# Performance work log

Measured on AMD Instinct MI355X. Metric: run time of the kernel, lower is better.

## Reference

```python
import jax, jax.numpy as jnp
import numpy as np

L, WIDTH, H, B, S = 3, 4, 512, 32, 512
NHW = 2
CIN = (WIDTH + 1) * H


def _windows(padded, off0):
    # padded: [B, S+2W, H] -> [B, S, (W+1)*H], window k covers padded[:, off0+k : off0+k+S]
    return jnp.concatenate([padded[:, off0 + k: off0 + k + S] for k in range(WIDTH + 1)], axis=-1)


def _highway(x, Ws, bs):
    # Ws: [NHW, H, 2H], bs: [NHW, 2H]. AllenNLP Highway: gate*x + (1-gate)*relu(nonlin)
    for j in range(NHW):
        proj = x @ Ws[j] + bs[j]
        nonlin, gate = jnp.split(proj, 2, axis=-1)
        g = jax.nn.sigmoid(gate)
        x = g * x + (1.0 - g) * jax.nn.relu(nonlin)
    return x


def setup_inputs() -> dict:
    key = jax.random.key(0)
    ks = jax.random.split(key, 13)
    inputs = jax.random.normal(ks[0], (B, S, H), dtype=jnp.float32)
    mask = jnp.ones((B, S), dtype=jnp.int32)
    fwd_pads = jax.random.normal(ks[1], (L, WIDTH, H), dtype=jnp.float32)
    bwd_pads = jax.random.normal(ks[2], (L, WIDTH, H), dtype=jnp.float32)
    fwd_W = jax.random.normal(ks[3], (L, CIN, H), dtype=jnp.float32) * 0.02
    bwd_W = jax.random.normal(ks[4], (L, CIN, H), dtype=jnp.float32) * 0.02
    fwd_b = jnp.zeros((L, H), dtype=jnp.float32)
    bwd_b = jnp.zeros((L, H), dtype=jnp.float32)
    fwd_hw_W = jax.random.normal(ks[5], (L, NHW, H, 2 * H), dtype=jnp.float32) * 0.04
    bwd_hw_W = jax.random.normal(ks[6], (L, NHW, H, 2 * H), dtype=jnp.float32) * 0.04
    fwd_hw_b = jnp.zeros((L, NHW, 2 * H), dtype=jnp.float32)
    bwd_hw_b = jnp.zeros((L, NHW, 2 * H), dtype=jnp.float32)
    return {"inputs": inputs, "mask": mask, "fwd_pads": fwd_pads, "bwd_pads": bwd_pads,
            "fwd_W": fwd_W, "fwd_b": fwd_b, "bwd_W": bwd_W, "bwd_b": bwd_b,
            "fwd_hw_W": fwd_hw_W, "fwd_hw_b": fwd_hw_b, "bwd_hw_W": bwd_hw_W, "bwd_hw_b": bwd_hw_b}


def reference(inputs, mask, fwd_pads, bwd_pads, fwd_W, fwd_b, bwd_W, bwd_b,
              fwd_hw_W, fwd_hw_b, bwd_hw_W, bwd_hw_b):
    f_seq = inputs
    b_seq = inputs
    outs = []
    for i in range(L):
        pf = jnp.broadcast_to(fwd_pads[i], (B, WIDTH, H))
        pb = jnp.broadcast_to(bwd_pads[i], (B, WIDTH, H))
        pad_f = jnp.concatenate([pf, f_seq, pb], axis=1)  # [B, S+2W, H]
        pad_b = jnp.concatenate([pf, b_seq, pb], axis=1)
        # forward windows start at offset 0 (positions t-W..t); backward at offset W (t..t+W)
        f_in = _windows(pad_f, 0)       # [B, S, (W+1)*H]
        b_in = _windows(pad_b, WIDTH)
        f = jax.nn.relu(f_in @ fwd_W[i] + fwd_b[i])
        f = _highway(f, fwd_hw_W[i], fwd_hw_b[i])
        b = jax.nn.relu(b_in @ bwd_W[i] + bwd_b[i])
        b = _highway(b, bwd_hw_W[i], bwd_hw_b[i])
        f_seq, b_seq = f, b
        outs.append(jnp.concatenate([f, b], axis=-1))
    return jnp.stack(outs, axis=0)  # [L, B, S, 2H]
```

## Files before the change

### kernel.cpp

```cpp
#include <hip/hip_runtime.h>
#include <hip/hip_fp16.h>
#include <cstdint>
#include <cstddef>

constexpr int HD   = 512;
constexpr int SQ   = 512;
constexpr int NB   = 32;
constexpr int LAY  = 3;
constexpr int WID  = 4;
constexpr int KIN  = (WID + 1) * HD;
constexpr int PROW = SQ + 2 * WID;
constexpr int MR   = NB * SQ;
constexpr int PSTR = NB * PROW * HD;

typedef _Float16 f16x8 __attribute__((ext_vector_type(8)));
typedef float    f32x4 __attribute__((ext_vector_type(4)));

__device__ __forceinline__ void gld16(void* lds, const void* g) {
  __builtin_amdgcn_global_load_lds(
      (__attribute__((address_space(1))) void*)(g),
      (__attribute__((address_space(3))) void*)(lds),
      16, 0, 0);
}

__global__ void transpose_w2(const float* __restrict__ inF, const float* __restrict__ inB,
                             _Float16* __restrict__ outF, _Float16* __restrict__ outB,
                             int R, int C, int nsl) {
  __shared__ float tile[32][33];
  const int z = blockIdx.z;
  const float* in = (z < nsl) ? inF : inB;
  _Float16* out   = (z < nsl) ? outF : outB;
  const int sl    = (z < nsl) ? z : z - nsl;
  const size_t base = (size_t)sl * R * C;
  const int r0 = blockIdx.y * 32, c0 = blockIdx.x * 32;
  const int tx = threadIdx.x, ty = threadIdx.y;
#pragma unroll
  for (int j = 0; j < 32; j += 8)
    tile[ty + j][tx] = in[base + (size_t)(r0 + ty + j) * C + (c0 + tx)];
  __syncthreads();
#pragma unroll
  for (int j = 0; j < 32; j += 8)
    out[base + (size_t)(c0 + ty + j) * R + (r0 + tx)] = (_Float16)tile[tx][ty + j];
}

__global__ void init_interior(const float4* __restrict__ in,
                              _Float16* __restrict__ padF, _Float16* __restrict__ padB) {
  const size_t idx = (size_t)blockIdx.x * 256 + threadIdx.x;
  float4 v = in[idx];
  const size_t e = idx * 4;
  const int h = (int)(e & (HD - 1));
  const size_t bt = e >> 9;
  const int t = (int)(bt & (SQ - 1));
  const int b = (int)(bt >> 9);
  const size_t o = ((size_t)(b * PROW + WID + t)) * HD + h;
  union { _Float16 hh[4]; uint2 u; } pk;
  pk.hh[0] = (_Float16)v.x; pk.hh[1] = (_Float16)v.y;
  pk.hh[2] = (_Float16)v.z; pk.hh[3] = (_Float16)v.w;
  *(uint2*)&padF[o] = pk.u;
  *(uint2*)&padB[o] = pk.u;
}

__global__ void fill_all_pads(const float* __restrict__ fpads, const float* __restrict__ bpads,
                              _Float16* __restrict__ padF, _Float16* __restrict__ padB) {
  const int idx = blockIdx.x * 256 + threadIdx.x;
  const int h  = idx & (HD - 1);
  const int w  = (idx >> 9) & 3;
  const int b  = (idx >> 11) & 31;
  const int fb = (idx >> 16) & 1;
  const int l  = idx >> 17;
  const float v = fb ? bpads[l * WID * HD + w * HD + h] : fpads[l * WID * HD + w * HD + h];
  const int row = fb ? (SQ + WID + w) : w;
  const size_t o = (size_t)l * PSTR + ((size_t)(b * PROW + row)) * HD + h;
  const _Float16 hv = (_Float16)v;
  padF[o] = hv;
  padB[o] = hv;
}

__global__ __launch_bounds__(256)
void conv_gemm(const _Float16* __restrict__ padFp, const _Float16* __restrict__ padBp,
               const _Float16* __restrict__ WtF, const _Float16* __restrict__ WtB,
               const float* __restrict__ biasF, const float* __restrict__ biasB,
               _Float16* __restrict__ tF, _Float16* __restrict__ tB) {
  const int id   = blockIdx.x;
  const int xcd  = id & 7;
  const int dir  = xcd >> 2;
  const int xl   = xcd & 3;
  const int slot = id >> 3;
  const int nt   = slot & 3;
  const int mg   = slot >> 2;
  const int mt   = xl + 4 * mg;

  const _Float16* pad = dir ? padBp : padFp;
  const _Float16* Wt  = dir ? WtB : WtF;
  const float* bias   = dir ? biasB : biasF;
  _Float16* outT      = dir ? tB : tF;
  const int off = dir ? WID : 0;

  const int m0 = mt * 128;
  const int n0 = nt * 128;
  const int b  = m0 >> 9;
  const int t0 = m0 & (SQ - 1);

  __shared__ alignas(16) _Float16 SM[128 * 128];
  _Float16* Asm = SM;
  _Float16* Bsm = SM + 8192;

  const int tid  = threadIdx.x;
  const int lane = tid & 63, wv = tid >> 6;
  const int wr = (wv >> 1) * 64, wc = (wv & 1) * 64;
  const int lr = lane & 15, q = lane >> 4;
  const int srow = tid >> 3;
  const int clog = (tid & 7) ^ (srow & 7);
  const int goff = clog * 8;

  f32x4 acc[4][4] = {};

  const size_t arow0 = (size_t)(b * PROW + t0 + off);

#pragma unroll 2
  for (int k0 = 0; k0 < KIN; k0 += 64) {
    const int kseg = k0 >> 9;
    const int h0 = k0 & (HD - 1);
    const _Float16* Ab = pad + (arow0 + kseg) * (size_t)HD + h0;
    const _Float16* Bb = Wt + (size_t)n0 * KIN + k0;
    __syncthreads();
#pragma unroll
    for (int j = 0; j < 4; ++j) {
      gld16(&Asm[j * 2048 + tid * 8], Ab + (size_t)(j * 32 + srow) * HD + goff);
      gld16(&Bsm[j * 2048 + tid * 8], Bb + (size_t)(j * 32 + srow) * KIN + goff);
    }
    __syncthreads();

#pragma unroll
    for (int h = 0; h < 2; ++h) {
      f16x8 af[4], bf[4];
      const int ch = ((h << 2) | q) ^ (lr & 7);
#pragma unroll
      for (int r = 0; r < 4; ++r)
        af[r] = *(const f16x8*)&Asm[(wr + r * 16 + lr) * 64 + ch * 8];
#pragma unroll
      for (int c = 0; c < 4; ++c)
        bf[c] = *(const f16x8*)&Bsm[(wc + c * 16 + lr) * 64 + ch * 8];
#pragma unroll
      for (int r = 0; r < 4; ++r)
#pragma unroll
        for (int c = 0; c < 4; ++c)
          acc[r][c] = __builtin_amdgcn_mfma_f32_16x16x32_f16(af[r], bf[c], acc[r][c], 0, 0, 0);
    }
  }

  __syncthreads();
#pragma unroll
  for (int c = 0; c < 4; ++c) {
    const int col = wc + c * 16 + lr;
    const float bv = bias[n0 + col];
#pragma unroll
    for (int r = 0; r < 4; ++r)
#pragma unroll
      for (int g = 0; g < 4; ++g) {
        const int row = wr + r * 16 + q * 4 + g;
        const int pc = (col >> 3) ^ (row & 7);
        float v = acc[r][c][g] + bv;
        v = v > 0.f ? v : 0.f;
        SM[row * 128 + pc * 8 + (col & 7)] = (_Float16)v;
      }
  }
  __syncthreads();
#pragma unroll
  for (int j = 0; j < 8; ++j) {
    const int cid = j * 256 + tid;
    const int row = cid >> 4;
    const int gc = cid & 15;
    const int pc = gc ^ (row & 7);
    f16x8 v8 = *(const f16x8*)&SM[row * 128 + pc * 8];
    *(f16x8*)&outT[(size_t)(m0 + row) * HD + n0 + gc * 8] = v8;
  }
}

__global__ __launch_bounds__(256)
void hw_gemm(const _Float16* __restrict__ xF, const _Float16* __restrict__ xB,
             const _Float16* __restrict__ WtFp, const _Float16* __restrict__ WtBp,
             const float* __restrict__ bFp, const float* __restrict__ bBp,
             _Float16* __restrict__ oFp, _Float16* __restrict__ oBp,
             float* __restrict__ out32, int mode) {
  const int id   = blockIdx.x;
  const int xcd  = id & 7;
  const int dir  = xcd >> 2;
  const int xl   = xcd & 3;
  const int slot = id >> 3;
  const int nt   = slot & 7;
  const int mg   = slot >> 3;
  const int mt   = xl + 4 * mg;

  const _Float16* x  = dir ? xB : xF;
  const _Float16* Wt = dir ? WtBp : WtFp;
  const float* bias  = dir ? bBp : bFp;
  _Float16* oh       = dir ? oBp : oFp;

  const int m0 = mt * 256;
  const int n0 = nt * 64;

  __shared__ alignas(16) _Float16 SM[32768];
  _Float16* Asm = SM;
  _Float16* Bn  = SM + 16384;
  _Float16* Bg  = SM + 20480;

  const int tid  = threadIdx.x;
  const int lane = tid & 63, wv = tid >> 6;
  const int lr = lane & 15, q = lane >> 4;
  const int srow = tid >> 3;
  const int clog = (tid & 7) ^ (srow & 7);
  const int goff = clog * 8;

  f32x4 an[4][4] = {};
  f32x4 ag[4][4] = {};

#pragma unroll 2
  for (int k0 = 0; k0 < HD; k0 += 64) {
    const _Float16* Ab  = x + (size_t)m0 * HD + k0;
    const _Float16* Bnb = Wt + (size_t)n0 * HD + k0;
    const _Float16* Bgb = Wt + (size_t)(HD + n0) * HD + k0;
    __syncthreads();
#pragma unroll
    for (int j = 0; j < 8; ++j)
      gld16(&Asm[j * 2048 + tid * 8], Ab + (size_t)(j * 32 + srow) * HD + goff);
#pragma unroll
    for (int j = 0; j < 2; ++j) {
      gld16(&Bn[j * 2048 + tid * 8], Bnb + (size_t)(j * 32 + srow) * HD + goff);
      gld16(&Bg[j * 2048 + tid * 8], Bgb + (size_t)(j * 32 + srow) * HD + goff);
    }
    __syncthreads();

#pragma unroll
    for (int h = 0; h < 2; ++h) {
      const int ch = ((h << 2) | q) ^ (lr & 7);
      f16x8 af[4], bn[4], bg[4];
#pragma unroll
      for (int r = 0; r < 4; ++r)
        af[r] = *(const f16x8*)&Asm[(wv * 64 + r * 16 + lr) * 64 + ch * 8];
#pragma unroll
      for (int c = 0; c < 4; ++c) {
        bn[c] = *(const f16x8*)&Bn[(c * 16 + lr) * 64 + ch * 8];
        bg[c] = *(const f16x8*)&Bg[(c * 16 + lr) * 64 + ch * 8];
      }
#pragma unroll
      for (int r = 0; r < 4; ++r)
#pragma unroll
        for (int c = 0; c < 4; ++c) {
          an[r][c] = __builtin_amdgcn_mfma_f32_16x16x32_f16(af[r], bn[c], an[r][c], 0, 0, 0);
          ag[r][c] = __builtin_amdgcn_mfma_f32_16x16x32_f16(af[r], bg[c], ag[r][c], 0, 0, 0);
        }
    }
  }

  __syncthreads();
#pragma unroll
  for (int c = 0; c < 4; ++c) {
    const int col = c * 16 + lr;
    const float bnv = bias[n0 + col];
    const float bgv = bias[HD + n0 + col];
#pragma unroll
    for (int r = 0; r < 4; ++r)
#pragma unroll
      for (int g = 0; g < 4; ++g) {
        const int row = wv * 64 + r * 16 + q * 4 + g;
        const int pc = (col >> 3) ^ (row & 7);
        const int a = row * 64 + pc * 8 + (col & 7);
        float nl = an[r][c][g] + bnv;
        nl = nl > 0.f ? nl : 0.f;
        SM[a] = (_Float16)nl;
        SM[16384 + a] = (_Float16)(ag[r][c][g] + bgv);
      }
  }
  __syncthreads();
#pragma unroll
  for (int j = 0; j < 8; ++j) {
    const int cid = j * 256 + tid;
    const int row = cid >> 3;
    const int gc = cid & 7;
    const int pc = gc ^ (row & 7);
    f16x8 nl8 = *(const f16x8*)&SM[row * 64 + pc * 8];
    f16x8 gz8 = *(const f16x8*)&SM[16384 + row * 64 + pc * 8];
    const int xrow = m0 + row;
    f16x8 xv8 = *(const f16x8*)&x[(size_t)xrow * HD + n0 + gc * 8];
    f16x8 o8;
    float of[8];
#pragma unroll
    for (int e = 0; e < 8; ++e) {
      const float gt = 1.f / (1.f + __expf(-(float)gz8[e]));
      const float o = gt * (float)xv8[e] + (1.f - gt) * (float)nl8[e];
      of[e] = o;
      o8[e] = (_Float16)o;
    }
    if (mode == 0) {
      *(f16x8*)&oh[(size_t)xrow * HD + n0 + gc * 8] = o8;
    } else {
      if (mode == 1) {
        const int bb = xrow >> 9, tt = xrow & (SQ - 1);
        *(f16x8*)&oh[((size_t)(bb * PROW + WID + tt)) * HD + n0 + gc * 8] = o8;
      }
      float* op = out32 + (size_t)xrow * (2 * HD) + dir * HD + n0 + gc * 8;
      *(float4*)op = make_float4(of[0], of[1], of[2], of[3]);
      *(float4*)(op + 4) = make_float4(of[4], of[5], of[6], of[7]);
    }
  }
}

extern "C" void kernel_launch(void* const* d_in, const int* in_sizes, int n_in,
                              void* d_out, int out_size, void* d_ws, size_t ws_size,
                              hipStream_t stream) {
  const float* inputs   = (const float*)d_in[0];
  const float* fwd_pads = (const float*)d_in[2];
  const float* bwd_pads = (const float*)d_in[3];
  const float* fwd_W    = (const float*)d_in[4];
  const float* fwd_b    = (const float*)d_in[5];
  const float* bwd_W    = (const float*)d_in[6];
  const float* bwd_b    = (const float*)d_in[7];
  const float* fwd_hw_W = (const float*)d_in[8];
  const float* fwd_hw_b = (const float*)d_in[9];
  const float* bwd_hw_W = (const float*)d_in[10];
  const float* bwd_hw_b = (const float*)d_in[11];
  float* out = (float*)d_out;

  char* p = (char*)d_ws;
  auto take = [&](size_t n) { char* r = p; p += (n + 255) & ~(size_t)255; return r; };

  _Float16* padF = (_Float16*)take((size_t)LAY * PSTR * 2);
  _Float16* padB = (_Float16*)take((size_t)LAY * PSTR * 2);
  _Float16* tF   = (_Float16*)take((size_t)MR * HD * 2);
  _Float16* tB   = (_Float16*)take((size_t)MR * HD * 2);
  _Float16* uF   = (_Float16*)take((size_t)MR * HD * 2);
  _Float16* uB   = (_Float16*)take((size_t)MR * HD * 2);
  _Float16* WtcF = (_Float16*)take((size_t)LAY * HD * KIN * 2);
  _Float16* WtcB = (_Float16*)take((size_t)LAY * HD * KIN * 2);
  _Float16* WthF = (_Float16*)take((size_t)LAY * 2 * (2 * HD) * HD * 2);
  _Float16* WthB = (_Float16*)take((size_t)LAY * 2 * (2 * HD) * HD * 2);

  transpose_w2<<<dim3(HD / 32, KIN / 32, 2 * LAY), dim3(32, 8), 0, stream>>>(
      fwd_W, bwd_W, WtcF, WtcB, KIN, HD, LAY);
  transpose_w2<<<dim3((2 * HD) / 32, HD / 32, 2 * LAY * 2), dim3(32, 8), 0, stream>>>(
      fwd_hw_W, bwd_hw_W, WthF, WthB, HD, 2 * HD, LAY * 2);

  init_interior<<<(NB * SQ * HD / 4) / 256, 256, 0, stream>>>((const float4*)inputs, padF, padB);
  fill_all_pads<<<(LAY * 2 * NB * WID * HD) / 256, 256, 0, stream>>>(fwd_pads, bwd_pads, padF, padB);

  for (int i = 0; i < LAY; ++i) {
    _Float16* pF = padF + (size_t)i * PSTR;
    _Float16* pB = padB + (size_t)i * PSTR;
    const int nx = (i + 1 < LAY) ? (i + 1) : 0;
    _Float16* nF = padF + (size_t)nx * PSTR;
    _Float16* nB = padB + (size_t)nx * PSTR;

    conv_gemm<<<dim3(1024), 256, 0, stream>>>(
        pF, pB,
        WtcF + (size_t)i * HD * KIN, WtcB + (size_t)i * HD * KIN,
        fwd_b + (size_t)i * HD, bwd_b + (size_t)i * HD, tF, tB);
    hw_gemm<<<dim3(1024), 256, 0, stream>>>(
        tF, tB,
        WthF + (size_t)(i * 2 + 0) * (2 * HD) * HD, WthB + (size_t)(i * 2 + 0) * (2 * HD) * HD,
        fwd_hw_b + (size_t)(i * 2 + 0) * (2 * HD), bwd_hw_b + (size_t)(i * 2 + 0) * (2 * HD),
        uF, uB, nullptr, 0);
    hw_gemm<<<dim3(1024), 256, 0, stream>>>(
        uF, uB,
        WthF + (size_t)(i * 2 + 1) * (2 * HD) * HD, WthB + (size_t)(i * 2 + 1) * (2 * HD) * HD,
        fwd_hw_b + (size_t)(i * 2 + 1) * (2 * HD), bwd_hw_b + (size_t)(i * 2 + 1) * (2 * HD),
        nF, nB, out + (size_t)i * MR * (2 * HD), (i + 1 < LAY) ? 1 : 2);
  }
}
```

Measured before the change: 983.3 us.

## Rewrite conv and highway GEMMs as 256x256 tiles with multi-stage async LDS pipeline

Both GEMM kernels now use 512-thread blocks computing 256x256 output tiles. A ring of eight 32-wide K sub-tiles in LDS is filled with async global-to-LDS loads, and explicit vmcnt waits and barriers overlap the loads with MFMA work, which also runs at raised wave priority. The highway weights are column-interleaved at transpose time so nonlinear and gate columns sit next to each other, letting one accumulator set cover both halves. This aims to raise arithmetic intensity and hide memory latency, at the cost of 128KB of LDS per block, fewer blocks, and fragile hand-written wait counts.

After: 899.4 us. 8.5% less time.

```diff
diff --git a/kernel.cpp b/kernel.cpp
--- a/kernel.cpp
+++ b/kernel.cpp
@@ -16,6 +16,10 @@
 typedef _Float16 f16x8 __attribute__((ext_vector_type(8)));
 typedef float    f32x4 __attribute__((ext_vector_type(4)));
 
+#define VMCNT(n) asm volatile("s_waitcnt vmcnt(" #n ")" ::: "memory")
+#define LGKM0()  asm volatile("s_waitcnt lgkmcnt(0)" ::: "memory")
+#define SBAR()   asm volatile("s_barrier" ::: "memory")
+
 __device__ __forceinline__ void gld16(void* lds, const void* g) {
   __builtin_amdgcn_global_load_lds(
       (__attribute__((address_space(1))) void*)(g),
@@ -23,9 +27,24 @@
       16, 0, 0);
 }
 
+__device__ __forceinline__ void stage_reg(_Float16* dst, const _Float16* src0,
+                                          int rstride, int tid) {
+#pragma unroll
+  for (int j = 0; j < 2; ++j) {
+    const int l = j * 512 + tid;
+    const int r = l >> 2;
+    const int c = ((l & 3) ^ ((r >> 1) & 3)) << 3;
+    gld16(dst + (size_t)l * 8, src0 + (size_t)r * rstride + c);
+  }
+}
+
+__device__ __forceinline__ f16x8 rdfrag(const _Float16* reg, int row, int q) {
+  return *(const f16x8*)&reg[row * 32 + ((q ^ ((row >> 1) & 3)) << 3)];
+}
+
 __global__ void transpose_w2(const float* __restrict__ inF, const float* __restrict__ inB,
                              _Float16* __restrict__ outF, _Float16* __restrict__ outB,
-                             int R, int C, int nsl) {
+                             int R, int C, int nsl, int ilv) {
   __shared__ float tile[32][33];
   const int z = blockIdx.z;
   const float* in = (z < nsl) ? inF : inB;
@@ -34,13 +53,17 @@
   const size_t base = (size_t)sl * R * C;
   const int r0 = blockIdx.y * 32, c0 = blockIdx.x * 32;
   const int tx = threadIdx.x, ty = threadIdx.y;
+  const int half = C >> 1;
 #pragma unroll
   for (int j = 0; j < 32; j += 8)
     tile[ty + j][tx] = in[base + (size_t)(r0 + ty + j) * C + (c0 + tx)];
   __syncthreads();
 #pragma unroll
-  for (int j = 0; j < 32; j += 8)
-    out[base + (size_t)(c0 + ty + j) * R + (r0 + tx)] = (_Float16)tile[tx][ty + j];
+  for (int j = 0; j < 32; j += 8) {
+    const int c = c0 + ty + j;
+    const int cc = ilv ? (((c & (half - 1)) << 1) | (c >= half ? 1 : 0)) : c;
+    out[base + (size_t)cc * R + (r0 + tx)] = (_Float16)tile[tx][ty + j];
+  }
 }
 
 __global__ void init_interior(const float4* __restrict__ in,
@@ -76,19 +99,19 @@
   padB[o] = hv;
 }
 
-__global__ __launch_bounds__(256)
+__global__ __launch_bounds__(512, 2)
 void conv_gemm(const _Float16* __restrict__ padFp, const _Float16* __restrict__ padBp,
                const _Float16* __restrict__ WtF, const _Float16* __restrict__ WtB,
                const float* __restrict__ biasF, const float* __restrict__ biasB,
                _Float16* __restrict__ tF, _Float16* __restrict__ tB) {
-  const int id   = blockIdx.x;
-  const int xcd  = id & 7;
-  const int dir  = xcd >> 2;
-  const int xl   = xcd & 3;
-  const int slot = id >> 3;
-  const int nt   = slot & 3;
-  const int mg   = slot >> 2;
-  const int mt   = xl + 4 * mg;
+  constexpr int NT = KIN / 64;
+  __shared__ alignas(16) _Float16 LDSA[65536];
+
+  const int id = blockIdx.x;
+  const int lg = (id & 7) * 32 + (id >> 3);
+  const int dir = lg >> 7;
+  const int nt  = (lg >> 6) & 1;
+  const int mt  = lg & 63;
 
   const _Float16* pad = dir ? padBp : padFp;
   const _Float16* Wt  = dir ? WtB : WtF;
@@ -96,210 +119,292 @@
   _Float16* outT      = dir ? tB : tF;
   const int off = dir ? WID : 0;
 
-  const int m0 = mt * 128;
-  const int n0 = nt * 128;
-  const int b  = m0 >> 9;
-  const int t0 = m0 & (SQ - 1);
-
-  __shared__ alignas(16) _Float16 SM[128 * 128];
-  _Float16* Asm = SM;
-  _Float16* Bsm = SM + 8192;
+  const int m0 = mt * 256, n0 = nt * 256;
+  const int b  = m0 >> 9, t0 = m0 & (SQ - 1);
+  const int arow0 = b * PROW + t0 + off;
 
   const int tid  = threadIdx.x;
   const int lane = tid & 63, wv = tid >> 6;
-  const int wr = (wv >> 1) * 64, wc = (wv & 1) * 64;
+  const int wm = wv >> 2, wn = wv & 3;
   const int lr = lane & 15, q = lane >> 4;
-  const int srow = tid >> 3;
-  const int clog = (tid & 7) ^ (srow & 7);
-  const int goff = clog * 8;
-
-  f32x4 acc[4][4] = {};
-
-  const size_t arow0 = (size_t)(b * PROW + t0 + off);
+
+  f32x4 acc[8][4] = {};
+
+  auto As = [&](int reg, int kk) {
+    const int kseg = kk >> 9, h0 = kk & (HD - 1);
+    stage_reg(LDSA + reg * 8192, pad + (size_t)(arow0 + kseg) * HD + h0, HD, tid);
+  };
+  auto Bs = [&](int reg, int kk) {
+    stage_reg(LDSA + reg * 8192, Wt + (size_t)n0 * KIN + kk, KIN, tid);
+  };
+
+  As(0, 0);  Bs(1, 0);  As(2, 32); Bs(3, 32);
+  As(4, 64); Bs(5, 64); As(6, 96);
 
 #pragma unroll 2
-  for (int k0 = 0; k0 < KIN; k0 += 64) {
-    const int kseg = k0 >> 9;
-    const int h0 = k0 & (HD - 1);
-    const _Float16* Ab = pad + (arow0 + kseg) * (size_t)HD + h0;
-    const _Float16* Bb = Wt + (size_t)n0 * KIN + k0;
-    __syncthreads();
-#pragma unroll
-    for (int j = 0; j < 4; ++j) {
-      gld16(&Asm[j * 2048 + tid * 8], Ab + (size_t)(j * 32 + srow) * HD + goff);
-      gld16(&Bsm[j * 2048 + tid * 8], Bb + (size_t)(j * 32 + srow) * KIN + goff);
-    }
-    __syncthreads();
-
-#pragma unroll
-    for (int h = 0; h < 2; ++h) {
-      f16x8 af[4], bf[4];
-      const int ch = ((h << 2) | q) ^ (lr & 7);
-#pragma unroll
-      for (int r = 0; r < 4; ++r)
-        af[r] = *(const f16x8*)&Asm[(wr + r * 16 + lr) * 64 + ch * 8];
-#pragma unroll
-      for (int c = 0; c < 4; ++c)
-        bf[c] = *(const f16x8*)&Bsm[(wc + c * 16 + lr) * 64 + ch * 8];
-#pragma unroll
-      for (int r = 0; r < 4; ++r)
-#pragma unroll
-        for (int c = 0; c < 4; ++c)
-          acc[r][c] = __builtin_amdgcn_mfma_f32_16x16x32_f16(af[r], bf[c], acc[r][c], 0, 0, 0);
-    }
-  }
-
-  __syncthreads();
-#pragma unroll
-  for (int c = 0; c < 4; ++c) {
-    const int col = wc + c * 16 + lr;
+  for (int kt = 0; kt < NT; ++kt) {
+    const int bf_ = (kt & 1) * 4, of_ = 4 - bf_;
+    const _Float16* A0 = LDSA + (bf_ + 0) * 8192;
+    const _Float16* B0 = LDSA + (bf_ + 1) * 8192;
+    const _Float16* A1 = LDSA + (bf_ + 2) * 8192;
+    const _Float16* B1 = LDSA + (bf_ + 3) * 8192;
+    const int k1 = (kt + 1 < NT ? kt + 1 : NT - 1) * 64;
+    const int k2 = (kt + 2 < NT ? kt + 2 : NT - 1) * 64;
+
+    f16x8 aF[8], bF[2];
+
+    VMCNT(10);
+    Bs(of_ + 3, k1 + 32);
+    SBAR();
+#pragma unroll
+    for (int mi = 0; mi < 8; ++mi) aF[mi] = rdfrag(A0, wm * 128 + mi * 16 + lr, q);
+#pragma unroll
+    for (int nj = 0; nj < 2; ++nj) bF[nj] = rdfrag(B0, wn * 64 + nj * 16 + lr, q);
+    __builtin_amdgcn_s_setprio(1);
+#pragma unroll
+    for (int mi = 0; mi < 8; ++mi)
+#pragma unroll
+      for (int nj = 0; nj < 2; ++nj)
+        acc[mi][nj] = __builtin_amdgcn_mfma_f32_16x16x32_f16(aF[mi], bF[nj], acc[mi][nj], 0, 0, 0);
+    __builtin_amdgcn_s_setprio(0);
+    LGKM0();
+    SBAR();
+
+    As(bf_ + 0, k2);
+    SBAR();
+#pragma unroll
+    for (int nj = 0; nj < 2; ++nj) bF[nj] = rdfrag(B0, wn * 64 + (nj + 2) * 16 + lr, q);
+    __builtin_amdgcn_s_setprio(1);
+#pragma unroll
+    for (int mi = 0; mi < 8; ++mi)
+#pragma unroll
+      for (int nj = 0; nj < 2; ++nj)
+        acc[mi][nj + 2] = __builtin_amdgcn_mfma_f32_16x16x32_f16(aF[mi], bF[nj], acc[mi][nj + 2], 0, 0, 0);
+    __builtin_amdgcn_s_setprio(0);
+    LGKM0();
+    SBAR();
+
+    VMCNT(10);
+    Bs(bf_ + 1, k2);
+    SBAR();
+#pragma unroll
+    for (int mi = 0; mi < 8; ++mi) aF[mi] = rdfrag(A1, wm * 128 + mi * 16 + lr, q);
+#pragma unroll
+    for (int nj = 0; nj < 2; ++nj) bF[nj] = rdfrag(B1, wn * 64 + nj * 16 + lr, q);
+    __builtin_amdgcn_s_setprio(1);
+#pragma unroll
+    for (int mi = 0; mi < 8; ++mi)
+#pragma unroll
+      for (int nj = 0; nj < 2; ++nj)
+        acc[mi][nj] = __builtin_amdgcn_mfma_f32_16x16x32_f16(aF[mi], bF[nj], acc[mi][nj], 0, 0, 0);
+    __builtin_amdgcn_s_setprio(0);
+    LGKM0();
+    SBAR();
+
+    As(bf_ + 2, k2 + 32);
+    SBAR();
+#pragma unroll
+    for (int nj = 0; nj < 2; ++nj) bF[nj] = rdfrag(B1, wn * 64 + (nj + 2) * 16 + lr, q);
+    __builtin_amdgcn_s_setprio(1);
+#pragma unroll
+    for (int mi = 0; mi < 8; ++mi)
+#pragma unroll
+      for (int nj = 0; nj < 2; ++nj)
+        acc[mi][nj + 2] = __builtin_amdgcn_mfma_f32_16x16x32_f16(aF[mi], bF[nj], acc[mi][nj + 2], 0, 0, 0);
+    __builtin_amdgcn_s_setprio(0);
+    LGKM0();
+    SBAR();
+  }
+
+  VMCNT(0);
+  SBAR();
+  _Float16* E = LDSA;
+#pragma unroll
+  for (int nj = 0; nj < 4; ++nj) {
+    const int col = wn * 64 + nj * 16 + lr;
     const float bv = bias[n0 + col];
 #pragma unroll
-    for (int r = 0; r < 4; ++r)
+    for (int mi = 0; mi < 8; ++mi)
 #pragma unroll
       for (int g = 0; g < 4; ++g) {
-        const int row = wr + r * 16 + q * 4 + g;
-        const int pc = (col >> 3) ^ (row & 7);
-        float v = acc[r][c][g] + bv;
+        const int row = wm * 128 + mi * 16 + q * 4 + g;
+        float v = acc[mi][nj][g] + bv;
         v = v > 0.f ? v : 0.f;
-        SM[row * 128 + pc * 8 + (col & 7)] = (_Float16)v;
+        E[row * 256 + col] = (_Float16)v;
       }
   }
-  __syncthreads();
-#pragma unroll
-  for (int j = 0; j < 8; ++j) {
-    const int cid = j * 256 + tid;
-    const int row = cid >> 4;
-    const int gc = cid & 15;
-    const int pc = gc ^ (row & 7);
-    f16x8 v8 = *(const f16x8*)&SM[row * 128 + pc * 8];
-    *(f16x8*)&outT[(size_t)(m0 + row) * HD + n0 + gc * 8] = v8;
-  }
-}
-
-__global__ __launch_bounds__(256)
+  LGKM0();
+  SBAR();
+#pragma unroll
+  for (int j = 0; j < 16; ++j) {
+    const int cid = j * 512 + tid;
+    const int row = cid >> 5, c = cid & 31;
+    f16x8 v8 = *(const f16x8*)&E[row * 256 + c * 8];
+    *(f16x8*)&outT[(size_t)(m0 + row) * HD + n0 + c * 8] = v8;
+  }
+}
+
+__global__ __launch_bounds__(512, 2)
 void hw_gemm(const _Float16* __restrict__ xF, const _Float16* __restrict__ xB,
              const _Float16* __restrict__ WtFp, const _Float16* __restrict__ WtBp,
              const float* __restrict__ bFp, const float* __restrict__ bBp,
              _Float16* __restrict__ oFp, _Float16* __restrict__ oBp,
              float* __restrict__ out32, int mode) {
-  const int id   = blockIdx.x;
-  const int xcd  = id & 7;
-  const int dir  = xcd >> 2;
-  const int xl   = xcd & 3;
-  const int slot = id >> 3;
-  const int nt   = slot & 7;
-  const int mg   = slot >> 3;
-  const int mt   = xl + 4 * mg;
+  constexpr int NT = HD / 64;
+  __shared__ alignas(16) _Float16 LDSA[65536];
+
+  const int id = blockIdx.x;
+  const int lg = (id & 7) * 64 + (id >> 3);
+  const int dir = lg >> 8;
+  const int r2  = lg & 255;
+  const int nt  = r2 >> 6, mt = r2 & 63;
 
   const _Float16* x  = dir ? xB : xF;
   const _Float16* Wt = dir ? WtBp : WtFp;
   const float* bias  = dir ? bBp : bFp;
   _Float16* oh       = dir ? oBp : oFp;
 
-  const int m0 = mt * 256;
-  const int n0 = nt * 64;
-
-  __shared__ alignas(16) _Float16 SM[32768];
-  _Float16* Asm = SM;
-  _Float16* Bn  = SM + 16384;
-  _Float16* Bg  = SM + 20480;
+  const int m0 = mt * 256, n0 = nt * 256;
 
   const int tid  = threadIdx.x;
   const int lane = tid & 63, wv = tid >> 6;
+  const int wm = wv >> 2, wn = wv & 3;
   const int lr = lane & 15, q = lane >> 4;
-  const int srow = tid >> 3;
-  const int clog = (tid & 7) ^ (srow & 7);
-  const int goff = clog * 8;
-
-  f32x4 an[4][4] = {};
-  f32x4 ag[4][4] = {};
+
+  f32x4 acc[8][4] = {};
+
+  auto As = [&](int reg, int kk) {
+    stage_reg(LDSA + reg * 8192, x + (size_t)m0 * HD + kk, HD, tid);
+  };
+  auto Bs = [&](int reg, int kk) {
+    stage_reg(LDSA + reg * 8192, Wt + (size_t)n0 * HD + kk, HD, tid);
+  };
+
+  As(0, 0);  Bs(1, 0);  As(2, 32); Bs(3, 32);
+  As(4, 64); Bs(5, 64); As(6, 96);
 
 #pragma unroll 2
-  for (int k0 = 0; k0 < HD; k0 += 64) {
-    const _Float16* Ab  = x + (size_t)m0 * HD + k0;
-    const _Float16* Bnb = Wt + (size_t)n0 * HD + k0;
-    const _Float16* Bgb = Wt + (size_t)(HD + n0) * HD + k0;
-    __syncthreads();
-#pragma unroll
-    for (int j = 0; j < 8; ++j)
-      gld16(&Asm[j * 2048 + tid * 8], Ab + (size_t)(j * 32 + srow) * HD + goff);
-#pragma unroll
-    for (int j = 0; j < 2; ++j) {
-      gld16(&Bn[j * 2048 + tid * 8], Bnb + (size_t)(j * 32 + srow) * HD + goff);
-      gld16(&Bg[j * 2048 + tid * 8], Bgb + (size_t)(j * 32 + srow) * HD + goff);
-    }
-    __syncthreads();
-
-#pragma unroll
-    for (int h = 0; h < 2; ++h) {
-      const int ch = ((h << 2) | q) ^ (lr & 7);
-      f16x8 af[4], bn[4], bg[4];
-#pragma unroll
-      for (int r = 0; r < 4; ++r)
-        af[r] = *(const f16x8*)&Asm[(wv * 64 + r * 16 + lr) * 64 + ch * 8];
-#pragma unroll
-      for (int c = 0; c < 4; ++c) {
-        bn[c] = *(const f16x8*)&Bn[(c * 16 + lr) * 64 + ch * 8];
-        bg[c] = *(const f16x8*)&Bg[(c * 16 + lr) * 64 + ch * 8];
+  for (int kt = 0; kt < NT; ++kt) {
+    const int bf_ = (kt & 1) * 4, of_ = 4 - bf_;
+    const _Float16* A0 = LDSA + (bf_ + 0) * 8192;
+    const _Float16* B0 = LDSA + (bf_ + 1) * 8192;
+    const _Float16* A1 = LDSA + (bf_ + 2) * 8192;
+    const _Float16* B1 = LDSA + (bf_ + 3) * 8192;
+    const int k1 = (kt + 1 < NT ? kt + 1 : NT - 1) * 64;
+    const int k2 = (kt + 2 < NT ? kt + 2 : NT - 1) * 64;
+
+    f16x8 aF[8], bF[2];
+
+    VMCNT(10);
+    Bs(of_ + 3, k1 + 32);
+    SBAR();
+#pragma unroll
+    for (int mi = 0; mi < 8; ++mi) aF[mi] = rdfrag(A0, wm * 128 + mi * 16 + lr, q);
+#pragma unroll
+    for (int nj = 0; nj < 2; ++nj) bF[nj] = rdfrag(B0, wn * 64 + nj * 16 + lr, q);
+    __builtin_amdgcn_s_setprio(1);
+#pragma unroll
+    for (int mi = 0; mi < 8; ++mi)
+#pragma unroll
+      for (int nj = 0; nj < 2; ++nj)
+        acc[mi][nj] = __builtin_amdgcn_mfma_f32_16x16x32_f16(aF[mi], bF[nj], acc[mi][nj], 0, 0, 0);
+    __builtin_amdgcn_s_setprio(0);
+    LGKM0();
+    SBAR();
+
+    As(bf_ + 0, k2);
+    SBAR();
+#pragma unroll
+    for (int nj = 0; nj < 2; ++nj) bF[nj] = rdfrag(B0, wn * 64 + (nj + 2) * 16 + lr, q);
+    __builtin_amdgcn_s_setprio(1);
+#pragma unroll
+    for (int mi = 0; mi < 8; ++mi)
+#pragma unroll
+      for (int nj = 0; nj < 2; ++nj)
+        acc[mi][nj + 2] = __builtin_amdgcn_mfma_f32_16x16x32_f16(aF[mi], bF[nj], acc[mi][nj + 2], 0, 0, 0);
+    __builtin_amdgcn_s_setprio(0);
+    LGKM0();
+    SBAR();
+
+    VMCNT(10);
+    Bs(bf_ + 1, k2);
+    SBAR();
+#pragma unroll
+    for (int mi = 0; mi < 8; ++mi) aF[mi] = rdfrag(A1, wm * 128 + mi * 16 + lr, q);
+#pragma unroll
+    for (int nj = 0; nj < 2; ++nj) bF[nj] = rdfrag(B1, wn * 64 + nj * 16 + lr, q);
+    __builtin_amdgcn_s_setprio(1);
+#pragma unroll
+    for (int mi = 0; mi < 8; ++mi)
+#pragma unroll
+      for (int nj = 0; nj < 2; ++nj)
+        acc[mi][nj] = __builtin_amdgcn_mfma_f32_16x16x32_f16(aF[mi], bF[nj], acc[mi][nj], 0, 0, 0);
+    __builtin_amdgcn_s_setprio(0);
+    LGKM0();
+    SBAR();
+
+    As(bf_ + 2, k2 + 32);
+    SBAR();
+#pragma unroll
+    for (int nj = 0; nj < 2; ++nj) bF[nj] = rdfrag(B1, wn * 64 + (nj + 2) * 16 + lr, q);
+    __builtin_amdgcn_s_setprio(1);
+#pragma unroll
+    for (int mi = 0; mi < 8; ++mi)
+#pragma unroll
+      for (int nj = 0; nj < 2; ++nj)
+        acc[mi][nj + 2] = __builtin_amdgcn_mfma_f32_16x16x32_f16(aF[mi], bF[nj], acc[mi][nj + 2], 0, 0, 0);
+    __builtin_amdgcn_s_setprio(0);
+    LGKM0();
+    SBAR();
+  }
+
+  VMCNT(0);
+  SBAR();
+  _Float16* E = LDSA;
+#pragma unroll
+  for (int nj = 0; nj < 4; ++nj) {
+    const int col = wn * 64 + nj * 16 + lr;
+    const int gcol = n0 + col;
+    const float bv = bias[((gcol & 1) << 9) + (gcol >> 1)];
+#pragma unroll
+    for (int mi = 0; mi < 8; ++mi)
+#pragma unroll
+      for (int g = 0; g < 4; ++g) {
+        const int row = wm * 128 + mi * 16 + q * 4 + g;
+        E[row * 256 + col] = (_Float16)(acc[mi][nj][g] + bv);
       }
-#pragma unroll
-      for (int r = 0; r < 4; ++r)
-#pragma unroll
-        for (int c = 0; c < 4; ++c) {
-          an[r][c] = __builtin_amdgcn_mfma_f32_16x16x32_f16(af[r], bn[c], an[r][c], 0, 0, 0);
-          ag[r][c] = __builtin_amdgcn_mfma_f32_16x16x32_f16(af[r], bg[c], ag[r][c], 0, 0, 0);
-        }
-    }
-  }
-
-  __syncthreads();
-#pragma unroll
-  for (int c = 0; c < 4; ++c) {
-    const int col = c * 16 + lr;
-    const float bnv = bias[n0 + col];
-    const float bgv = bias[HD + n0 + col];
-#pragma unroll
-    for (int r = 0; r < 4; ++r)
-#pragma unroll
-      for (int g = 0; g < 4; ++g) {
-        const int row = wv * 64 + r * 16 + q * 4 + g;
-        const int pc = (col >> 3) ^ (row & 7);
-        const int a = row * 64 + pc * 8 + (col & 7);
-        float nl = an[r][c][g] + bnv;
-        nl = nl > 0.f ? nl : 0.f;
-        SM[a] = (_Float16)nl;
-        SM[16384 + a] = (_Float16)(ag[r][c][g] + bgv);
-      }
-  }
-  __syncthreads();
+  }
+  LGKM0();
+  SBAR();
 #pragma unroll
   for (int j = 0; j < 8; ++j) {
-    const int cid = j * 256 + tid;
-    const int row = cid >> 3;
-    const int gc = cid & 7;
-    const int pc = gc ^ (row & 7);
-    f16x8 nl8 = *(const f16x8*)&SM[row * 64 + pc * 8];
-    f16x8 gz8 = *(const f16x8*)&SM[16384 + row * 64 + pc * 8];
+    const int cid = j * 512 + tid;
+    const int row = cid >> 4, pc = cid & 15;
+    f16x8 u = *(const f16x8*)&E[row * 256 + pc * 16];
+    f16x8 v = *(const f16x8*)&E[row * 256 + pc * 16 + 8];
     const int xrow = m0 + row;
-    f16x8 xv8 = *(const f16x8*)&x[(size_t)xrow * HD + n0 + gc * 8];
+    const int oc0 = (n0 >> 1) + pc * 8;
+    f16x8 xv8 = *(const f16x8*)&x[(size_t)xrow * HD + oc0];
     f16x8 o8;
     float of[8];
 #pragma unroll
     for (int e = 0; e < 8; ++e) {
-      const float gt = 1.f / (1.f + __expf(-(float)gz8[e]));
-      const float o = gt * (float)xv8[e] + (1.f - gt) * (float)nl8[e];
+      float nl = (e < 4) ? (float)u[2 * e]     : (float)v[2 * e - 8];
+      float gz = (e < 4) ? (float)u[2 * e + 1] : (float)v[2 * e - 7];
+      nl = nl > 0.f ? nl : 0.f;
+      const float gt = 1.f / (1.f + __expf(-gz));
+      const float o = gt * (float)xv8[e] + (1.f - gt) * nl;
       of[e] = o;
       o8[e] = (_Float16)o;
     }
     if (mode == 0) {
-      *(f16x8*)&oh[(size_t)xrow * HD + n0 + gc * 8] = o8;
+      *(f16x8*)&oh[(size_t)xrow * HD + oc0] = o8;
     } else {
       if (mode == 1) {
         const int bb = xrow >> 9, tt = xrow & (SQ - 1);
-        *(f16x8*)&oh[((size_t)(bb * PROW + WID + tt)) * HD + n0 + gc * 8] = o8;
+        *(f16x8*)&oh[((size_t)(bb * PROW + WID + tt)) * HD + oc0] = o8;
       }
-      float* op = out32 + (size_t)xrow * (2 * HD) + dir * HD + n0 + gc * 8;
+      float* op = out32 + (size_t)xrow * (2 * HD) + dir * HD + oc0;
       *(float4*)op = make_float4(of[0], of[1], of[2], of[3]);
       *(float4*)(op + 4) = make_float4(of[4], of[5], of[6], of[7]);
     }
@@ -337,9 +442,9 @@
   _Float16* WthB = (_Float16*)take((size_t)LAY * 2 * (2 * HD) * HD * 2);
 
   transpose_w2<<<dim3(HD / 32, KIN / 32, 2 * LAY), dim3(32, 8), 0, stream>>>(
-      fwd_W, bwd_W, WtcF, WtcB, KIN, HD, LAY);
+      fwd_W, bwd_W, WtcF, WtcB, KIN, HD, LAY, 0);
   transpose_w2<<<dim3((2 * HD) / 32, HD / 32, 2 * LAY * 2), dim3(32, 8), 0, stream>>>(
-      fwd_hw_W, bwd_hw_W, WthF, WthB, HD, 2 * HD, LAY * 2);
+      fwd_hw_W, bwd_hw_W, WthF, WthB, HD, 2 * HD, LAY * 2, 1);
 
   init_interior<<<(NB * SQ * HD / 4) / 256, 256, 0, stream>>>((const float4*)inputs, padF, padB);
   fill_all_pads<<<(LAY * 2 * NB * WID * HD) / 256, 256, 0, stream>>>(fwd_pads, bwd_pads, padF, padB);
@@ -351,16 +456,16 @@
     _Float16* nF = padF + (size_t)nx * PSTR;
     _Float16* nB = padB + (size_t)nx * PSTR;
 
-    conv_gemm<<<dim3(1024), 256, 0, stream>>>(
+    conv_gemm<<<dim3(256), dim3(512), 0, stream>>>(
         pF, pB,
         WtcF + (size_t)i * HD * KIN, WtcB + (size_t)i * HD * KIN,
         fwd_b + (size_t)i * HD, bwd_b + (size_t)i * HD, tF, tB);
-    hw_gemm<<<dim3(1024), 256, 0, stream>>>(
+    hw_gemm<<<dim3(512), dim3(512), 0, stream>>>(
         tF, tB,
         WthF + (size_t)(i * 2 + 0) * (2 * HD) * HD, WthB + (size_t)(i * 2 + 0) * (2 * HD) * HD,
         fwd_hw_b + (size_t)(i * 2 + 0) * (2 * HD), bwd_hw_b + (size_t)(i * 2 + 0) * (2 * HD),
         uF, uB, nullptr, 0);
-    hw_gemm<<<dim3(1024), 256, 0, stream>>>(
+    hw_gemm<<<dim3(512), dim3(512), 0, stream>>>(
         uF, uB,
         WthF + (size_t)(i * 2 + 1) * (2 * HD) * HD, WthB + (size_t)(i * 2 + 1) * (2 * HD) * HD,
         fwd_hw_b + (size_t)(i * 2 + 1) * (2 * HD), bwd_hw_b + (size_t)(i * 2 + 1) * (2 * HD),
```
